# Kernel tuning notes

Measured on AMD Instinct MI355X. Metric: run time of the kernel, lower is better.

Reference implementation:

```python
import jax, jax.numpy as jnp
import numpy as np

N, R, DIN, DOUT = 4096, 16, 256, 256


def setup_inputs() -> dict:
    key = jax.random.key(0)
    k1, k2, k3, k4 = jax.random.split(key, 4)
    x = jax.random.normal(k1, (N, DIN), dtype=jnp.float32)
    relations = jax.random.randint(k2, (N,), 0, R, dtype=jnp.int32)
    # kaiming-uniform-ish init for w, uniform bound for bias (as in reset_parameters)
    bound = 1.0 / np.sqrt(DIN).astype(np.float32)
    w = jax.random.uniform(k3, (R, DIN, DOUT), dtype=jnp.float32, minval=-bound, maxval=bound)
    bias = jax.random.uniform(k4, (R, DOUT), dtype=jnp.float32, minval=-bound, maxval=bound)
    return {"x": x, "relations": relations, "w": w, "bias": bias}


def reference(x, relations, w, bias):
    # out[n] = x[n] @ w[relations[n]] + bias[relations[n]]
    w_g = jnp.take(w, relations, axis=0)          # [N, DIN, DOUT] gathered per-row weights
    out = jnp.einsum('ni,nio->no', x, w_g)        # per-sample matmul
    out = out + jnp.take(bias, relations, axis=0)  # [N, DOUT]
    return out
```

## Files before the change

kernel.cpp:

```cpp
#include <hip/hip_runtime.h>

#define R_REL 16
#define DIN   256
#define DOUT  256
#define BM    32
#define GX    16
#define CHUNK 128

typedef __attribute__((ext_vector_type(4))) float f32x4;
typedef __attribute__((ext_vector_type(8))) short s16x8;
typedef unsigned long long u64;

__device__ __forceinline__ short f2bf(float f) {
    union { float f; unsigned u; } v; v.f = f;
    unsigned r = v.u + 0x7FFFu + ((v.u >> 16) & 1u);
    return (short)(r >> 16);
}

#define MFMA(a, b, c) __builtin_amdgcn_mfma_f32_16x16x32_bf16(a, b, c, 0, 0, 0)

__global__ __launch_bounds__(256) void fused_kernel(
        const float* __restrict__ x, const int* __restrict__ rel,
        const float* __restrict__ w, const float* __restrict__ bias,
        float* __restrict__ out) {
    const int r    = blockIdx.y;
    const int ch   = blockIdx.z;
    const int t    = threadIdx.x;
    const int lane = t & 63, wv = t >> 6;
    const int frow = lane & 15, kgrp = lane >> 4;

    __shared__ int    wcnt[65];
    __shared__ int    rowidx[BM];
    __shared__ ushort A[BM][264];
    __shared__ ushort Bc[2][CHUNK][40];

    int myrel[16];
    #pragma unroll
    for (int it = 0; it < 16; ++it)
        myrel[it] = rel[wv * 1024 + it * 64 + lane];

    #pragma unroll
    for (int it = 0; it < 16; ++it) {
        const u64 m = __ballot(myrel[it] == r);
        if (lane == 0) wcnt[wv * 16 + it] = (int)__popcll(m);
    }
    __syncthreads();
    if (wv == 0) {
        int c = wcnt[lane];
        const int orig = c;
        #pragma unroll
        for (int d = 1; d < 64; d <<= 1) {
            const int u = __shfl_up(c, d);
            if (lane >= d) c += u;
        }
        wcnt[lane] = c - orig;
        if (lane == 63) wcnt[64] = c;
    }
    __syncthreads();
    const int count = wcnt[64];

    const int col0 = ch * CHUNK;
    const int colw = col0 + wv * 32;
    const float bv0 = bias[r * DOUT + colw + frow];
    const float bv1 = bias[r * DOUT + colw + 16 + frow];

    const u64 ltmask = (1ull << lane) - 1ull;
    const int half  = t >> 7;
    const int colr  = t & 127;
    const float* wcol = w + (size_t)r * DIN * DOUT + col0 + colr;

    for (int tile = blockIdx.x; tile * BM < count; tile += GX) {
        const int row0 = tile * BM;
        __syncthreads();

        if (t < BM && row0 + t >= count) rowidx[t] = 0;
        #pragma unroll
        for (int it = 0; it < 16; ++it) {
            const bool match = (myrel[it] == r);
            const u64 m = __ballot(match);
            if (match) {
                const int rank = wcnt[wv * 16 + it] + (int)__popcll(m & ltmask);
                const int s = rank - row0;
                if (s >= 0 && s < BM) rowidx[s] = wv * 1024 + it * 64 + lane;
            }
        }
        __syncthreads();

        {
            const int rl = t >> 3, seg = t & 7;
            const float* src = x + (size_t)rowidx[rl] * DIN + seg * 32;
            #pragma unroll
            for (int q = 0; q < 4; ++q) {
                const f32x4 v0 = *(const f32x4*)(src + q * 8);
                const f32x4 v1 = *(const f32x4*)(src + q * 8 + 4);
                s16x8 o;
                o[0]=f2bf(v0[0]); o[1]=f2bf(v0[1]); o[2]=f2bf(v0[2]); o[3]=f2bf(v0[3]);
                o[4]=f2bf(v1[0]); o[5]=f2bf(v1[1]); o[6]=f2bf(v1[2]); o[7]=f2bf(v1[3]);
                *(s16x8*)&A[rl][seg * 32 + q * 8] = o;
            }
        }

        float g[16];
        #pragma unroll
        for (int i = 0; i < 16; ++i)
            g[i] = wcol[(size_t)(half * 16 + i) * DOUT];

        f32x4 acc[2][2] = {};
        #pragma unroll
        for (int ks = 0; ks < 8; ++ks) {
            s16x8 o0, o1;
            #pragma unroll
            for (int i = 0; i < 8; ++i) { o0[i] = f2bf(g[i]); o1[i] = f2bf(g[8 + i]); }
            {
                ushort* dst = &Bc[ks & 1][colr][half * 16];
                *(s16x8*)dst       = o0;
                *(s16x8*)(dst + 8) = o1;
            }
            float gn[16];
            if (ks < 7) {
                #pragma unroll
                for (int i = 0; i < 16; ++i)
                    gn[i] = wcol[(size_t)((ks + 1) * 32 + half * 16 + i) * DOUT];
            }
            __syncthreads();

            const s16x8 af0 = *(const s16x8*)&A[frow][ks * 32 + kgrp * 8];
            const s16x8 af1 = *(const s16x8*)&A[16 + frow][ks * 32 + kgrp * 8];
            const s16x8 bf0 = *(const s16x8*)&Bc[ks & 1][wv * 32 + frow][kgrp * 8];
            const s16x8 bf1 = *(const s16x8*)&Bc[ks & 1][wv * 32 + 16 + frow][kgrp * 8];
            acc[0][0] = MFMA(af0, bf0, acc[0][0]);
            acc[1][0] = MFMA(af1, bf0, acc[1][0]);
            acc[0][1] = MFMA(af0, bf1, acc[0][1]);
            acc[1][1] = MFMA(af1, bf1, acc[1][1]);

            if (ks < 7) {
                #pragma unroll
                for (int i = 0; i < 16; ++i) g[i] = gn[i];
            }
        }

        #pragma unroll
        for (int n = 0; n < 2; ++n) {
            const int col = colw + n * 16 + frow;
            const float bv = n ? bv1 : bv0;
            #pragma unroll
            for (int m = 0; m < 2; ++m) {
                #pragma unroll
                for (int v = 0; v < 4; ++v) {
                    const int rl = m * 16 + kgrp * 4 + v;
                    if (row0 + rl < count)
                        out[(size_t)rowidx[rl] * DOUT + col] = acc[m][n][v] + bv;
                }
            }
        }
    }
}

extern "C" void kernel_launch(void* const* d_in, const int* in_sizes, int n_in,
                              void* d_out, int out_size, void* d_ws, size_t ws_size,
                              hipStream_t stream) {
    const float* x    = (const float*)d_in[0];
    const int*   rel  = (const int*)  d_in[1];
    const float* w    = (const float*)d_in[2];
    const float* bias = (const float*)d_in[3];
    float*       out  = (float*)d_out;

    dim3 grid(GX, R_REL, 2);
    fused_kernel<<<grid, 256, 0, stream>>>(x, rel, w, bias, out);
}
```

Before: 17.93 us.

## Keep full-K weight slab resident in LDS and narrow output chunk

```diff
diff --git a/kernel.cpp b/kernel.cpp
--- a/kernel.cpp
+++ b/kernel.cpp
@@ -4,12 +4,16 @@
 #define DIN   256
 #define DOUT  256
 #define BM    32
-#define GX    16
-#define CHUNK 128
+#define GX    12
+#define CHUNK 64
+#define NCH   (DOUT / CHUNK)
 
 typedef __attribute__((ext_vector_type(4))) float f32x4;
+typedef __attribute__((ext_vector_type(4))) int   i32x4;
 typedef __attribute__((ext_vector_type(8))) short s16x8;
 typedef unsigned long long u64;
+
+#define MFMA(a, b, c) __builtin_amdgcn_mfma_f32_16x16x32_bf16(a, b, c, 0, 0, 0)
 
 __device__ __forceinline__ short f2bf(float f) {
     union { float f; unsigned u; } v; v.f = f;
@@ -17,7 +21,9 @@
     return (short)(r >> 16);
 }
 
-#define MFMA(a, b, c) __builtin_amdgcn_mfma_f32_16x16x32_bf16(a, b, c, 0, 0, 0)
+__device__ __forceinline__ int swz(int rc, int k) {
+    return rc * 256 + (k ^ ((rc & 7) << 3));
+}
 
 __global__ __launch_bounds__(256) void fused_kernel(
         const float* __restrict__ x, const int* __restrict__ rel,
@@ -31,128 +37,124 @@
 
     __shared__ int    wcnt[65];
     __shared__ int    rowidx[BM];
-    __shared__ ushort A[BM][264];
-    __shared__ ushort Bc[2][CHUNK][40];
+    __shared__ ushort A [BM * 256];
+    __shared__ ushort Bc[CHUNK * 256];
 
-    int myrel[16];
+    i32x4 mr[4];
+    {
+        const i32x4* rp = (const i32x4*)(rel + t * 16);
+        #pragma unroll
+        for (int i = 0; i < 4; ++i) mr[i] = rp[i];
+    }
     #pragma unroll
-    for (int it = 0; it < 16; ++it)
-        myrel[it] = rel[wv * 1024 + it * 64 + lane];
-
-    #pragma unroll
-    for (int it = 0; it < 16; ++it) {
-        const u64 m = __ballot(myrel[it] == r);
-        if (lane == 0) wcnt[wv * 16 + it] = (int)__popcll(m);
-    }
+    for (int i = 0; i < 4; ++i)
+        #pragma unroll
+        for (int j = 0; j < 4; ++j) {
+            const u64 m = __ballot(mr[i][j] == r);
+            if (lane == 0) wcnt[wv * 16 + i * 4 + j] = (int)__popcll(m);
+        }
     __syncthreads();
     if (wv == 0) {
         int c = wcnt[lane];
         const int orig = c;
         #pragma unroll
         for (int d = 1; d < 64; d <<= 1) {
-            const int u = __shfl_up(c, d);
-            if (lane >= d) c += u;
+            const int u_ = __shfl_up(c, d);
+            if (lane >= d) c += u_;
         }
         wcnt[lane] = c - orig;
         if (lane == 63) wcnt[64] = c;
     }
     __syncthreads();
     const int count = wcnt[64];
+    if (blockIdx.x * BM >= count) return;
 
     const int col0 = ch * CHUNK;
-    const int colw = col0 + wv * 32;
-    const float bv0 = bias[r * DOUT + colw + frow];
-    const float bv1 = bias[r * DOUT + colw + 16 + frow];
+    const int c4   = (t & 15) * 4;
+    const int kb   = (t >> 4) * 16;
+    const float* wp = w + ((size_t)r * DIN + kb) * DOUT + col0 + c4;
+    f32x4 g[16];
+    #pragma unroll
+    for (int i = 0; i < 16; ++i)
+        g[i] = *(const f32x4*)(wp + (size_t)i * DOUT);
 
     const u64 ltmask = (1ull << lane) - 1ull;
-    const int half  = t >> 7;
-    const int colr  = t & 127;
-    const float* wcol = w + (size_t)r * DIN * DOUT + col0 + colr;
+    const int colg = col0 + wv * 16 + frow;
+    const float bv = bias[r * DOUT + colg];
 
+    bool first = true;
     for (int tile = blockIdx.x; tile * BM < count; tile += GX) {
         const int row0 = tile * BM;
-        __syncthreads();
+        if (!first) __syncthreads();
 
         if (t < BM && row0 + t >= count) rowidx[t] = 0;
         #pragma unroll
-        for (int it = 0; it < 16; ++it) {
-            const bool match = (myrel[it] == r);
-            const u64 m = __ballot(match);
-            if (match) {
-                const int rank = wcnt[wv * 16 + it] + (int)__popcll(m & ltmask);
-                const int s = rank - row0;
-                if (s >= 0 && s < BM) rowidx[s] = wv * 1024 + it * 64 + lane;
+        for (int i = 0; i < 4; ++i)
+            #pragma unroll
+            for (int j = 0; j < 4; ++j) {
+                const bool match = (mr[i][j] == r);
+                const u64 m = __ballot(match);
+                if (match) {
+                    const int s = wcnt[wv * 16 + i * 4 + j]
+                                + (int)__popcll(m & ltmask) - row0;
+                    if (s >= 0 && s < BM) rowidx[s] = t * 16 + i * 4 + j;
+                }
             }
+        __syncthreads();
+
+        const int arow = t >> 3, aseg = t & 7;
+        const float* ax = x + (size_t)rowidx[arow] * DIN + aseg * 32;
+        f32x4 av[8];
+        #pragma unroll
+        for (int q = 0; q < 8; ++q) av[q] = *(const f32x4*)(ax + q * 4);
+
+        if (first) {
+            first = false;
+            #pragma unroll
+            for (int j = 0; j < 4; ++j) {
+                s16x8 o0, o1;
+                #pragma unroll
+                for (int i = 0; i < 8; ++i) {
+                    o0[i] = f2bf(g[i][j]);
+                    o1[i] = f2bf(g[8 + i][j]);
+                }
+                const int c = c4 + j;
+                *(s16x8*)&Bc[swz(c, kb)]     = o0;
+                *(s16x8*)&Bc[swz(c, kb + 8)] = o1;
+            }
+        }
+        #pragma unroll
+        for (int q = 0; q < 4; ++q) {
+            s16x8 o;
+            #pragma unroll
+            for (int j = 0; j < 4; ++j) {
+                o[j]     = f2bf(av[2 * q][j]);
+                o[4 + j] = f2bf(av[2 * q + 1][j]);
+            }
+            *(s16x8*)&A[swz(arow, aseg * 32 + q * 8)] = o;
         }
         __syncthreads();
 
-        {
-            const int rl = t >> 3, seg = t & 7;
-            const float* src = x + (size_t)rowidx[rl] * DIN + seg * 32;
-            #pragma unroll
-            for (int q = 0; q < 4; ++q) {
-                const f32x4 v0 = *(const f32x4*)(src + q * 8);
-                const f32x4 v1 = *(const f32x4*)(src + q * 8 + 4);
-                s16x8 o;
-                o[0]=f2bf(v0[0]); o[1]=f2bf(v0[1]); o[2]=f2bf(v0[2]); o[3]=f2bf(v0[3]);
-                o[4]=f2bf(v1[0]); o[5]=f2bf(v1[1]); o[6]=f2bf(v1[2]); o[7]=f2bf(v1[3]);
-                *(s16x8*)&A[rl][seg * 32 + q * 8] = o;
-            }
-        }
-
-        float g[16];
-        #pragma unroll
-        for (int i = 0; i < 16; ++i)
-            g[i] = wcol[(size_t)(half * 16 + i) * DOUT];
-
-        f32x4 acc[2][2] = {};
+        f32x4 acc0 = {}, acc1 = {};
         #pragma unroll
         for (int ks = 0; ks < 8; ++ks) {
-            s16x8 o0, o1;
-            #pragma unroll
-            for (int i = 0; i < 8; ++i) { o0[i] = f2bf(g[i]); o1[i] = f2bf(g[8 + i]); }
-            {
-                ushort* dst = &Bc[ks & 1][colr][half * 16];
-                *(s16x8*)dst       = o0;
-                *(s16x8*)(dst + 8) = o1;
-            }
-            float gn[16];
-            if (ks < 7) {
-                #pragma unroll
-                for (int i = 0; i < 16; ++i)
-                    gn[i] = wcol[(size_t)((ks + 1) * 32 + half * 16 + i) * DOUT];
-            }
-            __syncthreads();
-
-            const s16x8 af0 = *(const s16x8*)&A[frow][ks * 32 + kgrp * 8];
-            const s16x8 af1 = *(const s16x8*)&A[16 + frow][ks * 32 + kgrp * 8];
-            const s16x8 bf0 = *(const s16x8*)&Bc[ks & 1][wv * 32 + frow][kgrp * 8];
-            const s16x8 bf1 = *(const s16x8*)&Bc[ks & 1][wv * 32 + 16 + frow][kgrp * 8];
-            acc[0][0] = MFMA(af0, bf0, acc[0][0]);
-            acc[1][0] = MFMA(af1, bf0, acc[1][0]);
-            acc[0][1] = MFMA(af0, bf1, acc[0][1]);
-            acc[1][1] = MFMA(af1, bf1, acc[1][1]);
-
-            if (ks < 7) {
-                #pragma unroll
-                for (int i = 0; i < 16; ++i) g[i] = gn[i];
-            }
+            const int ke = ks * 32 + kgrp * 8;
+            const s16x8 af0 = *(const s16x8*)&A[swz(frow, ke)];
+            const s16x8 af1 = *(const s16x8*)&A[swz(frow + 16, ke)];
+            const s16x8 bf  = *(const s16x8*)&Bc[swz(wv * 16 + frow, ke)];
+            acc0 = MFMA(af0, bf, acc0);
+            acc1 = MFMA(af1, bf, acc1);
         }
 
         #pragma unroll
-        for (int n = 0; n < 2; ++n) {
-            const int col = colw + n * 16 + frow;
-            const float bv = n ? bv1 : bv0;
+        for (int m = 0; m < 2; ++m)
             #pragma unroll
-            for (int m = 0; m < 2; ++m) {
-                #pragma unroll
-                for (int v = 0; v < 4; ++v) {
-                    const int rl = m * 16 + kgrp * 4 + v;
-                    if (row0 + rl < count)
-                        out[(size_t)rowidx[rl] * DOUT + col] = acc[m][n][v] + bv;
-                }
+            for (int v = 0; v < 4; ++v) {
+                const int s = m * 16 + kgrp * 4 + v;
+                if (row0 + s < count)
+                    out[(size_t)rowidx[s] * DOUT + colg] =
+                        (m ? acc1[v] : acc0[v]) + bv;
             }
-        }
     }
 }
 
@@ -165,6 +167,6 @@
     const float* bias = (const float*)d_in[3];
     float*       out  = (float*)d_out;
 
-    dim3 grid(GX, R_REL, 2);
+    dim3 grid(GX, R_REL, NCH);
     fused_kernel<<<grid, 256, 0, stream>>>(x, rel, w, bias, out);
 }
```

After: 16.95 us. -5.5%, faster.
